# Optimization experiments

Measured on AMD Instinct MI355X. Metric: run time of the kernel, lower is better.

Reference implementation:

```python
import jax, jax.numpy as jnp
import numpy as np

NLAT_IN, NLON_IN = 360, 720
NLAT_OUT, NLON_OUT = 180, 360
KERNEL_SIZE = 3
THETA_CUTOFF = KERNEL_SIZE * np.pi / NLAT_IN  # default theta_cutoff
B, C = 2, 64


def _cc_lats_weights(n):
    # Clenshaw-Curtis quadrature on [-1,1] (torch-harmonics 'equiangular' grid);
    # latitudes (colatitude) = arccos(nodes) = pi*k/(n-1) in [0, pi].
    N = n - 1
    theta = np.pi * np.arange(n) / N
    w = np.ones(n)
    for j in range(1, N // 2 + 1):
        b = 1.0 if 2 * j == N else 2.0
        w -= b * np.cos(2.0 * j * theta) / (4.0 * j * j - 1.0)
    w *= 2.0 / N
    w[0] *= 0.5
    w[-1] *= 0.5
    return theta, w


def _precompute_psi():
    # Mirrors _precompute_convolution_tensor + _compute_support_vals_isotropic.
    d_theta = THETA_CUTOFF / KERNEL_SIZE
    lats_in, _ = _cc_lats_weights(NLAT_IN)
    lats_out, _ = _cc_lats_weights(NLAT_OUT)
    phis = np.linspace(0.0, 2.0 * np.pi, NLON_IN)
    alpha = -lats_in[None, :, None].astype(np.float32)   # [1, H, 1]
    beta = phis[None, None, :].astype(np.float32)        # [1, 1, W]
    gamma = lats_out[:, None, None].astype(np.float32)   # [T, 1, 1]
    z = np.cos(alpha) * np.cos(gamma) - np.cos(beta) * np.sin(alpha) * np.sin(gamma)
    with np.errstate(invalid="ignore"):
        theta = np.arccos(z)  # [T, H, W]; nan where |z|>1 (excluded by mask, as in torch)
    segs, lats, lons, vals = [], [], [], []
    for ik in range(KERNEL_SIZE):
        itheta = ik * d_theta
        with np.errstate(invalid="ignore"):
            mask = (np.abs(theta - itheta) < d_theta) & (theta < THETA_CUTOFF)
        t_idx, h_idx, w_idx = np.nonzero(mask)
        segs.append(ik * NLAT_OUT + t_idx)  # fused (kernel, nlat_out) segment id
        lats.append(h_idx)
        lons.append(w_idx)
        vals.append(1.0 - np.abs(theta[mask] - itheta) / d_theta)
    return (np.concatenate(segs).astype(np.int32),
            np.concatenate(lats).astype(np.int32),
            np.concatenate(lons).astype(np.int32),
            np.concatenate(vals).astype(np.float32))


def setup_inputs() -> dict:
    key = jax.random.key(0)
    x = jax.random.normal(key, (B, C, NLAT_IN, NLON_IN), dtype=jnp.float32)
    _, wgl = _cc_lats_weights(NLAT_IN)
    quad_weights = jnp.asarray(2.0 * np.pi * wgl[:, None] / NLON_IN, dtype=jnp.float32)
    seg, lat, lon, val = _precompute_psi()
    return {"x": x, "quad_weights": quad_weights,
            "psi_seg": jnp.asarray(seg), "psi_lat": jnp.asarray(lat),
            "psi_lon": jnp.asarray(lon), "psi_val": jnp.asarray(val)}


def reference(x, quad_weights, psi_seg, psi_lat, psi_lon, psi_val):
    # out[b,c,k,t,p] = sum_{(k,t,h,w) in psi} val * qw[h] * x[b,c,h,(w-(p+1)*s) mod W]
    Bx, Cx, H, W = x.shape
    scale = W // NLON_OUT  # longitudinal shift per output longitude (torch.roll step)
    xw = (quad_weights * x).reshape(Bx * Cx, H, W)  # [BC, H, W]
    num_seg = KERNEL_SIZE * NLAT_OUT

    def step(carry, p):
        cols = (psi_lon - (p + 1) * scale) % W                 # rolled longitude per nnz
        g = xw[:, psi_lat, cols] * psi_val                     # [BC, nnz] gather + scale
        out_p = jax.ops.segment_sum(g.T, psi_seg, num_segments=num_seg)  # [K*T, BC]
        return carry, out_p

    _, ys = jax.lax.scan(step, None, jnp.arange(NLON_OUT))     # [P, K*T, BC]
    out = ys.transpose(2, 1, 0).reshape(Bx, Cx, KERNEL_SIZE, NLAT_OUT, NLON_OUT)
    return out
```

## Files before the change

### kernel.cpp

```cpp
#include <hip/hip_runtime.h>


#define NLAT_IN  360
#define NLON_IN  720
#define NLAT_OUT 180
#define NLON_OUT 360
#define KSIZE    3
#define NSEG     (KSIZE * NLAT_OUT)
#define CHW      (NLAT_IN * NLON_IN)
#define BCTOT    128
#define G        4
#define NBCG     (BCTOT / G)
#define MAXR     2
#define PH       10
#define NTHREADS 256
#define SLOTS    432
#define MIRROR   (SLOTS - NLON_OUT)
#define ROWB     (SLOTS * 16)

typedef float v2f __attribute__((ext_vector_type(2)));

__device__ __forceinline__ void PKF(v2f& a, v2f x, v2f c) {
    asm("v_pk_fma_f32 %0, %1, %2, %0" : "+v"(a) : "v"(x), "v"(c));
}


__global__ void prep1_kernel(const int* __restrict__ seg, const int* __restrict__ lat,
                             const float* __restrict__ val, int nnz,
                             int* __restrict__ ptrh, int* __restrict__ hbase,
                             int* __restrict__ hlast, int* __restrict__ flags) {
    int idx = blockIdx.x * blockDim.x + threadIdx.x;
    if (idx >= NSEG * PH) return;
    int s = idx / PH, j = idx - s * PH;
    int lo = 0, hi = nnz;
    while (lo < hi) { int m = (lo + hi) >> 1; if (seg[m] < s) lo = m + 1; else hi = m; }
    int e0 = lo;
    lo = e0; hi = nnz;
    while (lo < hi) { int m = (lo + hi) >> 1; if (seg[m] < s + 1) lo = m + 1; else hi = m; }
    int e1 = lo;
    if (e0 >= e1) {
        ptrh[idx] = e0; flags[idx] = 0;
        if (j == 0) { hbase[s] = 1 << 28; hlast[s] = -(1 << 28); }
        return;
    }
    int hb = lat[e0];
    if (j == 0) { hbase[s] = hb; hlast[s] = lat[e1 - 1]; }
    int a;
    { int tg = hb + j; lo = e0; hi = e1;
      while (lo < hi) { int m = (lo + hi) >> 1; if (lat[m] < tg) lo = m + 1; else hi = m; }
      a = lo; }
    ptrh[idx] = a;
    int f = 0;
    if (j < PH - 1) {
        int tg = hb + j + 1; lo = a; hi = e1;
        while (lo < hi) { int m = (lo + hi) >> 1; if (lat[m] < tg) lo = m + 1; else hi = m; }
        int b = lo;
        if (b - a == NLON_IN) {
            float v0 = val[a], v1 = val[a + 240], v2 = val[a + 480];
            float d = fmaxf(fabsf(v0 - v1), fmaxf(fabsf(v0 - v2), fabsf(v1 - v2)));
            f = (d < 1e-5f) ? 1 : 0;
        }
    }
    flags[idx] = f;
}

__global__ void cf_kernel(const int* __restrict__ lat, const float* __restrict__ val,
                          const float* __restrict__ qw, int nnz, float* __restrict__ cfb) {
    int e = blockIdx.x * blockDim.x + threadIdx.x;
    if (e < nnz) cfb[e] = val[e] * qw[lat[e]];
}

__global__ void runs_kernel(const int* __restrict__ lon, const int* __restrict__ ptrh,
                            const int* __restrict__ flags,
                            int* __restrict__ runcnt, uint2* __restrict__ runslab) {
    const int idx  = blockIdx.x * 4 + (threadIdx.x >> 6);
    if (idx >= NSEG * PH) return;
    const int lane = threadIdx.x & 63;
    const int j = idx % PH;
    int runbase = 0;
    if (j < PH - 1) {
        const int a = ptrh[idx], b = ptrh[idx + 1];
        if (b > a && !flags[idx]) {
            for (int c = a; c < b; c += 64) {
                const int e = c + lane;
                const bool active = e < b;
                const int w   = active ? lon[e] : 0;
                const int wm1 = (active && e > a) ? lon[e - 1] : -99;
                const bool isStart = active && (lane == 0 || w != wm1 + 1);
                const unsigned long long mask = __ballot(isStart);
                if (isStart) {
                    const int cnt = min(64, b - c);
                    unsigned long long hv = (mask >> lane) >> 1;
                    const int len = hv ? __ffsll((long long)hv) : (cnt - lane);
                    const int cidx = __popcll(mask & ((1ull << lane) - 1ull));
                    const int s0 = ((w >> 1) + NLON_OUT - 1) % NLON_OUT;
                    runslab[a + runbase + cidx] = make_uint2(
                        (unsigned)e, (unsigned)(s0 | ((w & 1) << 9) | (len << 11)));
                }
                runbase += __popcll(mask);
            }
        }
    }
    if (lane == 0) runcnt[idx] = runbase;
}


__global__ __launch_bounds__(NTHREADS) void disco_kernel(
    const float* __restrict__ x,
    const float* __restrict__ cfb,
    const uint2* __restrict__ runslab,
    const int*   __restrict__ runcnt,
    const int*   __restrict__ ptrh,
    const int*   __restrict__ hbase,
    const int*   __restrict__ hlast,
    const int*   __restrict__ flags,
    float*       __restrict__ out)
{
    __shared__ float4 ldsx[MAXR * 2][SLOTS];
    __shared__ v2f    accbuf[120][6];

    const int tid      = threadIdx.x;
    const int lane     = tid & 63;
    const int wpair    = tid >> 7;
    const int pairlane = tid & 127;
    const int pid      = (pairlane < 120) ? pairlane : pairlane - 120;
    const int p0       = 3 * pid;
    const int bc0      = blockIdx.x * G;
    const int ty       = blockIdx.y;
    const int t        = (ty & 1) ? (NLAT_OUT - 1 - (ty >> 1)) : (ty >> 1);
    const int s        = blockIdx.z * NLAT_OUT + t;
    const int hb = hbase[s], hl = hlast[s];

    v2f a0l = {0.f, 0.f}, a0h = a0l, a1l = a0l, a1h = a0l, a2l = a0l, a2h = a0l;
    const char* lb = (const char*)&ldsx[0][0];

    for (int r0 = hb; r0 <= hl; r0 += MAXR) {
        const int rn = min(MAXR, hl - r0 + 1);
        __syncthreads();
        for (int r = 0; r < rn; ++r) {
            const float* xr = x + (size_t)bc0 * CHW + (size_t)(r0 + r) * NLON_IN;
            for (int m = tid; m < NLON_OUT; m += NTHREADS) {
                const float2 v0 = *(const float2*)(xr + 2 * m);
                const float2 v1 = *(const float2*)(xr + 2 * m + CHW);
                const float2 v2 = *(const float2*)(xr + 2 * m + 2 * CHW);
                const float2 v3 = *(const float2*)(xr + 2 * m + 3 * CHW);
                const float4 ev = {v0.x, v1.x, v2.x, v3.x};
                const float4 ov = {v0.y, v1.y, v2.y, v3.y};
                ldsx[2 * r + 0][m] = ev;
                ldsx[2 * r + 1][m] = ov;
                if (m < MIRROR) {
                    ldsx[2 * r + 0][NLON_OUT + m] = ev;
                    ldsx[2 * r + 1][NLON_OUT + m] = ov;
                }
            }
        }
        __syncthreads();
        for (int r = 0; r < rn; ++r) {
            const int j = (r0 + r) - hb;
            if (j < 0 || j >= PH - 1) continue;
            if ((j & 1) != wpair) continue;
            const int idx = s * PH + j;
            const int a = ptrh[idx], b = ptrh[idx + 1];
            if (a >= b) continue;
            const int rp0 = (j & 1) * 2;
            if (flags[idx]) {
                float4 v = {0.f, 0.f, 0.f, 0.f};
                for (int m = lane; m < NLON_OUT; m += 64) {
                    const float4 u0 = ldsx[rp0][m], u1 = ldsx[rp0 + 1][m];
                    v.x += u0.x + u1.x; v.y += u0.y + u1.y;
                    v.z += u0.z + u1.z; v.w += u0.w + u1.w;
                }
#pragma unroll
                for (int o = 32; o >= 1; o >>= 1) {
                    v.x += __shfl_xor(v.x, o); v.y += __shfl_xor(v.y, o);
                    v.z += __shfl_xor(v.z, o); v.w += __shfl_xor(v.w, o);
                }
                const float cf = cfb[a];
                a0l.x = fmaf(cf, v.x, a0l.x); a0l.y = fmaf(cf, v.y, a0l.y);
                a0h.x = fmaf(cf, v.z, a0h.x); a0h.y = fmaf(cf, v.w, a0h.y);
                a1l.x = fmaf(cf, v.x, a1l.x); a1l.y = fmaf(cf, v.y, a1l.y);
                a1h.x = fmaf(cf, v.z, a1h.x); a1h.y = fmaf(cf, v.w, a1h.y);
                a2l.x = fmaf(cf, v.x, a2l.x); a2l.y = fmaf(cf, v.y, a2l.y);
                a2h.x = fmaf(cf, v.z, a2h.x); a2h.y = fmaf(cf, v.w, a2h.y);
                continue;
            }
            const int rc = runcnt[idx];
            for (int rr = 0; rr < rc; ++rr) {
                const uint2 R = runslab[a + rr];
                const int e0  = __builtin_amdgcn_readfirstlane((int)R.x);
                const int y   = __builtin_amdgcn_readfirstlane((int)R.y);
                const int s0A = y & 511;
                const int odd = (y >> 9) & 1;
                const int len = y >> 11;
                int qA = s0A - p0 - 2; qA += (qA >> 31) & NLON_OUT;
                const char* baseA = lb + (size_t)(rp0 + odd) * ROWB + ((size_t)qA << 4);
                const char* baseB = lb + (size_t)(rp0 + (odd ^ 1)) * ROWB
                                       + ((size_t)(qA + odd) << 4);
                const float* cfp = cfb + e0;
                int i = 0;
                if (len >= 8) {
                    v2f A0l = *(const v2f*)(baseA +  0), A0h = *(const v2f*)(baseA +  8);
                    v2f A1l = *(const v2f*)(baseA + 16), A1h = *(const v2f*)(baseA + 24);
                    v2f A2l = *(const v2f*)(baseA + 32), A2h = *(const v2f*)(baseA + 40);
                    v2f B0l = *(const v2f*)(baseB +  0), B0h = *(const v2f*)(baseB +  8);
                    v2f B1l = *(const v2f*)(baseB + 16), B1h = *(const v2f*)(baseB + 24);
                    v2f B2l = *(const v2f*)(baseB + 32), B2h = *(const v2f*)(baseB + 40);
                    v2f A3l, A3h, B3l, B3h;
                    const char* ldA = baseA + 48;
                    const char* ldB = baseB + 48;
                    for (; i + 8 <= len; i += 8) {
                        float cs; v2f c;
                        A3l = *(const v2f*)(ldA); A3h = *(const v2f*)(ldA + 8); ldA += 16;
                        cs = cfp[i + 0]; c = (v2f){cs, cs};
                        PKF(a2l, A0l, c); PKF(a2h, A0h, c);
                        PKF(a1l, A1l, c); PKF(a1h, A1h, c);
                        PKF(a0l, A2l, c); PKF(a0h, A2h, c);
                        B3l = *(const v2f*)(ldB); B3h = *(const v2f*)(ldB + 8); ldB += 16;
                        cs = cfp[i + 1]; c = (v2f){cs, cs};
                        PKF(a2l, B0l, c); PKF(a2h, B0h, c);
                        PKF(a1l, B1l, c); PKF(a1h, B1h, c);
                        PKF(a0l, B2l, c); PKF(a0h, B2h, c);
                        A0l = *(const v2f*)(ldA); A0h = *(const v2f*)(ldA + 8); ldA += 16;
                        cs = cfp[i + 2]; c = (v2f){cs, cs};
                        PKF(a2l, A1l, c); PKF(a2h, A1h, c);
                        PKF(a1l, A2l, c); PKF(a1h, A2h, c);
                        PKF(a0l, A3l, c); PKF(a0h, A3h, c);
                        B0l = *(const v2f*)(ldB); B0h = *(const v2f*)(ldB + 8); ldB += 16;
                        cs = cfp[i + 3]; c = (v2f){cs, cs};
                        PKF(a2l, B1l, c); PKF(a2h, B1h, c);
                        PKF(a1l, B2l, c); PKF(a1h, B2h, c);
                        PKF(a0l, B3l, c); PKF(a0h, B3h, c);
                        A1l = *(const v2f*)(ldA); A1h = *(const v2f*)(ldA + 8); ldA += 16;
                        cs = cfp[i + 4]; c = (v2f){cs, cs};
                        PKF(a2l, A2l, c); PKF(a2h, A2h, c);
                        PKF(a1l, A3l, c); PKF(a1h, A3h, c);
                        PKF(a0l, A0l, c); PKF(a0h, A0h, c);
                        B1l = *(const v2f*)(ldB); B1h = *(const v2f*)(ldB + 8); ldB += 16;
                        cs = cfp[i + 5]; c = (v2f){cs, cs};
                        PKF(a2l, B2l, c); PKF(a2h, B2h, c);
                        PKF(a1l, B3l, c); PKF(a1h, B3h, c);
                        PKF(a0l, B0l, c); PKF(a0h, B0h, c);
                        A2l = *(const v2f*)(ldA); A2h = *(const v2f*)(ldA + 8); ldA += 16;
                        cs = cfp[i + 6]; c = (v2f){cs, cs};
                        PKF(a2l, A3l, c); PKF(a2h, A3h, c);
                        PKF(a1l, A0l, c); PKF(a1h, A0h, c);
                        PKF(a0l, A1l, c); PKF(a0h, A1h, c);
                        B2l = *(const v2f*)(ldB); B2h = *(const v2f*)(ldB + 8); ldB += 16;
                        cs = cfp[i + 7]; c = (v2f){cs, cs};
                        PKF(a2l, B3l, c); PKF(a2h, B3h, c);
                        PKF(a1l, B0l, c); PKF(a1h, B0h, c);
                        PKF(a0l, B1l, c); PKF(a0h, B1h, c);
                    }
                }
                for (; i < len; ++i) {
                    const int m = i >> 1;
                    const char* bp = (i & 1) ? (baseB + ((size_t)m << 4))
                                             : (baseA + ((size_t)m << 4));
                    const float cs = cfp[i]; const v2f c = (v2f){cs, cs};
                    const v2f w0l = *(const v2f*)(bp +  0), w0h = *(const v2f*)(bp +  8);
                    const v2f w1l = *(const v2f*)(bp + 16), w1h = *(const v2f*)(bp + 24);
                    const v2f w2l = *(const v2f*)(bp + 32), w2h = *(const v2f*)(bp + 40);
                    PKF(a2l, w0l, c); PKF(a2h, w0h, c);
                    PKF(a1l, w1l, c); PKF(a1h, w1h, c);
                    PKF(a0l, w2l, c); PKF(a0h, w2h, c);
                }
            }
        }
    }

    __syncthreads();
    if (wpair == 1 && pairlane < 120) {
        accbuf[pid][0] = a0l; accbuf[pid][1] = a0h;
        accbuf[pid][2] = a1l; accbuf[pid][3] = a1h;
        accbuf[pid][4] = a2l; accbuf[pid][5] = a2h;
    }
    __syncthreads();
    if (wpair == 0 && pairlane < 120) {
        a0l += accbuf[pid][0]; a0h += accbuf[pid][1];
        a1l += accbuf[pid][2]; a1h += accbuf[pid][3];
        a2l += accbuf[pid][4]; a2h += accbuf[pid][5];
        const size_t cs_ = (size_t)NSEG * NLON_OUT;
        const size_t ob  = ((size_t)bc0 * NSEG + s) * NLON_OUT + p0;
        out[ob]              = a0l.x; out[ob + 1]              = a1l.x; out[ob + 2]              = a2l.x;
        out[ob + cs_]        = a0l.y; out[ob + cs_ + 1]        = a1l.y; out[ob + cs_ + 2]        = a2l.y;
        out[ob + 2 * cs_]    = a0h.x; out[ob + 2 * cs_ + 1]    = a1h.x; out[ob + 2 * cs_ + 2]    = a2h.x;
        out[ob + 3 * cs_]    = a0h.y; out[ob + 3 * cs_ + 1]    = a1h.y; out[ob + 3 * cs_ + 2]    = a2h.y;
    }
}


__global__ void segptr_kernel(const int* __restrict__ seg, int nnz, int* __restrict__ ptr) {
    int s = blockIdx.x * blockDim.x + threadIdx.x;
    if (s > NSEG) return;
    if (s == NSEG) { ptr[NSEG] = nnz; return; }
    int lo = 0, hi = nnz;
    while (lo < hi) { int m = (lo + hi) >> 1; if (seg[m] < s) lo = m + 1; else hi = m; }
    ptr[s] = lo;
}

__global__ __launch_bounds__(384) void disco_simple_kernel(
    const float* __restrict__ x, const float* __restrict__ qw,
    const int* __restrict__ lat, const int* __restrict__ lon,
    const float* __restrict__ val, const int* __restrict__ ptr,
    float* __restrict__ out)
{
    const int p = threadIdx.x;
    if (p >= NLON_OUT) return;
    const int kt = blockIdx.x, bc0 = blockIdx.y * 8;
    const int e0 = ptr[kt], e1 = ptr[kt + 1];
    float acc[8];
#pragma unroll
    for (int g = 0; g < 8; ++g) acc[g] = 0.0f;
    const int pw = 2 * p + 2;
    const float* xb = x + (size_t)bc0 * CHW;
    for (int e = e0; e < e1; ++e) {
        const int h = lat[e], w = lon[e];
        const float cf = val[e] * qw[h];
        int col = w - pw; if (col < 0) col += NLON_IN;
        const float* src = xb + h * NLON_IN + col;
#pragma unroll
        for (int g = 0; g < 8; ++g) acc[g] = fmaf(cf, src[(size_t)g * CHW], acc[g]);
    }
    const size_t ob = ((size_t)bc0 * NSEG + kt) * NLON_OUT + p;
#pragma unroll
    for (int g = 0; g < 8; ++g) out[ob + (size_t)g * NSEG * NLON_OUT] = acc[g];
}


extern "C" void kernel_launch(void* const* d_in, const int* in_sizes, int n_in,
                              void* d_out, int out_size, void* d_ws, size_t ws_size,
                              hipStream_t stream)
{
    const float* x   = (const float*)d_in[0];
    const float* qw  = (const float*)d_in[1];
    const int*   seg = (const int*)  d_in[2];
    const int*   lat = (const int*)  d_in[3];
    const int*   lon = (const int*)  d_in[4];
    const float* val = (const float*)d_in[5];
    const int    nnz = in_sizes[2];
    const int    nnzpad = (nnz + 3) & ~3;

    char* w = (char*)d_ws;
    size_t off = 0;
    int* ptrh   = (int*)(w + off); off += (size_t)NSEG * PH * 4;
    int* hbase  = (int*)(w + off); off += NSEG * 4;
    int* hlast  = (int*)(w + off); off += NSEG * 4;
    int* flags  = (int*)(w + off); off += (size_t)NSEG * PH * 4;
    int* runcnt = (int*)(w + off); off += (size_t)NSEG * PH * 4;
    float* cfb  = (float*)(w + off); off += (size_t)nnzpad * 4;
    off = (off + 7) & ~(size_t)7;
    uint2* runslab = (uint2*)(w + off); off += (size_t)nnz * 8;

    if (ws_size < off) {
        int* ptr = (int*)d_ws;
        segptr_kernel<<<(NSEG + 1 + 255) / 256, 256, 0, stream>>>(seg, nnz, ptr);
        dim3 grid(NSEG, BCTOT / 8);
        disco_simple_kernel<<<grid, 384, 0, stream>>>(x, qw, lat, lon, val, ptr,
                                                      (float*)d_out);
        return;
    }

    prep1_kernel<<<(NSEG * PH + 255) / 256, 256, 0, stream>>>(seg, lat, val, nnz,
                                                              ptrh, hbase, hlast, flags);
    cf_kernel<<<(nnz + 255) / 256, 256, 0, stream>>>(lat, val, qw, nnz, cfb);
    runs_kernel<<<(NSEG * PH + 3) / 4, 256, 0, stream>>>(lon, ptrh, flags,
                                                         runcnt, runslab);

    dim3 grid(NBCG, NLAT_OUT, KSIZE);
    disco_kernel<<<grid, NTHREADS, 0, stream>>>(x, cfb, runslab, runcnt,
                                                ptrh, hbase, hlast, flags,
                                                (float*)d_out);
}
```

Baseline: 183.2 us.

## Prefetch next row pair into registers while computing current rows

Global loads of input rows are moved into registers (sv0/sv1/sv2) and issued for the next MAXR row pair before the compute phase on the current pair, then written to LDS after the next barrier. The per-row loop is flattened so 720 elements across two rows are covered by three fixed per-thread slots. This hides global memory latency behind the FMA loop. The cost is extra register pressure from 24 prefetch floats, which may reduce occupancy.

```diff
diff --git a/kernel.cpp b/kernel.cpp
--- a/kernel.cpp
+++ b/kernel.cpp
@@ -17,6 +17,7 @@
 #define SLOTS    432
 #define MIRROR   (SLOTS - NLON_OUT)
 #define ROWB     (SLOTS * 16)
+#define SWI      3
 
 typedef float v2f __attribute__((ext_vector_type(2)));
 
@@ -134,135 +135,200 @@
     v2f a0l = {0.f, 0.f}, a0h = a0l, a1l = a0l, a1h = a0l, a2l = a0l, a2h = a0l;
     const char* lb = (const char*)&ldsx[0][0];
 
-    for (int r0 = hb; r0 <= hl; r0 += MAXR) {
-        const int rn = min(MAXR, hl - r0 + 1);
-        __syncthreads();
-        for (int r = 0; r < rn; ++r) {
-            const float* xr = x + (size_t)bc0 * CHW + (size_t)(r0 + r) * NLON_IN;
-            for (int m = tid; m < NLON_OUT; m += NTHREADS) {
-                const float2 v0 = *(const float2*)(xr + 2 * m);
-                const float2 v1 = *(const float2*)(xr + 2 * m + CHW);
-                const float2 v2 = *(const float2*)(xr + 2 * m + 2 * CHW);
-                const float2 v3 = *(const float2*)(xr + 2 * m + 3 * CHW);
-                const float4 ev = {v0.x, v1.x, v2.x, v3.x};
-                const float4 ov = {v0.y, v1.y, v2.y, v3.y};
-                ldsx[2 * r + 0][m] = ev;
-                ldsx[2 * r + 1][m] = ov;
-                if (m < MIRROR) {
-                    ldsx[2 * r + 0][NLON_OUT + m] = ev;
-                    ldsx[2 * r + 1][NLON_OUT + m] = ov;
+    float2 sv0[4], sv1[4], sv2[4];
+    const float* xb = x + (size_t)bc0 * CHW;
+
+#define LOADW(R0)                                                              \
+    {                                                                          \
+        {   const int idx_ = tid;                     \
+            const int rr_ = idx_ >= 360;                                       \
+            const int m_  = idx_ - 360 * rr_;                                  \
+            const int row_ = min((R0) + rr_, hl);                              \
+            const float* xr_ = xb + (size_t)row_ * NLON_IN + 2 * m_;           \
+            sv0[0] = *(const float2*)(xr_);                                    \
+            sv0[1] = *(const float2*)(xr_ + CHW);                              \
+            sv0[2] = *(const float2*)(xr_ + 2 * CHW);                          \
+            sv0[3] = *(const float2*)(xr_ + 3 * CHW);                          \
+        }                                                                      \
+        {   const int idx_ = tid + 256;               \
+            const int rr_ = idx_ >= 360;                                       \
+            const int m_  = idx_ - 360 * rr_;                                  \
+            const int row_ = min((R0) + rr_, hl);                              \
+            const float* xr_ = xb + (size_t)row_ * NLON_IN + 2 * m_;           \
+            sv1[0] = *(const float2*)(xr_);                                    \
+            sv1[1] = *(const float2*)(xr_ + CHW);                              \
+            sv1[2] = *(const float2*)(xr_ + 2 * CHW);                          \
+            sv1[3] = *(const float2*)(xr_ + 3 * CHW);                          \
+        }                                                                      \
+        if (tid < 208) {                                 \
+            const int idx_ = tid + 512;                                        \
+            const int rr_ = 1;                                                 \
+            const int m_  = idx_ - 360;                                        \
+            const int row_ = min((R0) + rr_, hl);                              \
+            const float* xr_ = xb + (size_t)row_ * NLON_IN + 2 * m_;           \
+            sv2[0] = *(const float2*)(xr_);                                    \
+            sv2[1] = *(const float2*)(xr_ + CHW);                              \
+            sv2[2] = *(const float2*)(xr_ + 2 * CHW);                          \
+            sv2[3] = *(const float2*)(xr_ + 3 * CHW);                          \
+        }                                                                      \
+    }
+
+#define WRITEW()                                                               \
+    {                                                                          \
+        {   const int idx_ = tid;                                              \
+            const int rr_ = idx_ >= 360;                                       \
+            const int m_  = idx_ - 360 * rr_;                                  \
+            const float4 ev_ = {sv0[0].x, sv0[1].x, sv0[2].x, sv0[3].x};       \
+            const float4 ov_ = {sv0[0].y, sv0[1].y, sv0[2].y, sv0[3].y};       \
+            ldsx[2 * rr_ + 0][m_] = ev_;                                       \
+            ldsx[2 * rr_ + 1][m_] = ov_;                                       \
+            if (m_ < MIRROR) {                                                 \
+                ldsx[2 * rr_ + 0][NLON_OUT + m_] = ev_;                        \
+                ldsx[2 * rr_ + 1][NLON_OUT + m_] = ov_;                        \
+            }                                                                  \
+        }                                                                      \
+        {   const int idx_ = tid + 256;                                        \
+            const int rr_ = idx_ >= 360;                                       \
+            const int m_  = idx_ - 360 * rr_;                                  \
+            const float4 ev_ = {sv1[0].x, sv1[1].x, sv1[2].x, sv1[3].x};       \
+            const float4 ov_ = {sv1[0].y, sv1[1].y, sv1[2].y, sv1[3].y};       \
+            ldsx[2 * rr_ + 0][m_] = ev_;                                       \
+            ldsx[2 * rr_ + 1][m_] = ov_;                                       \
+            if (m_ < MIRROR) {                                                 \
+                ldsx[2 * rr_ + 0][NLON_OUT + m_] = ev_;                        \
+                ldsx[2 * rr_ + 1][NLON_OUT + m_] = ov_;                        \
+            }                                                                  \
+        }                                                                      \
+        if (tid < 208) {                                                       \
+            const int m_ = tid + 512 - 360;                                    \
+            const float4 ev_ = {sv2[0].x, sv2[1].x, sv2[2].x, sv2[3].x};       \
+            const float4 ov_ = {sv2[0].y, sv2[1].y, sv2[2].y, sv2[3].y};       \
+            ldsx[2][m_] = ev_;                                                 \
+            ldsx[3][m_] = ov_;                                                 \
+            if (m_ < MIRROR) {                                                 \
+                ldsx[2][NLON_OUT + m_] = ev_;                                  \
+                ldsx[3][NLON_OUT + m_] = ov_;                                  \
+            }                                                                  \
+        }                                                                      \
+    }
+
+    if (hb <= hl) {
+        LOADW(hb);
+        for (int r0 = hb; r0 <= hl; r0 += MAXR) {
+            const int rn = min(MAXR, hl - r0 + 1);
+            __syncthreads();
+            WRITEW();
+            if (r0 + MAXR <= hl) LOADW(r0 + MAXR);
+            __syncthreads();
+            for (int r = 0; r < rn; ++r) {
+                const int j = (r0 + r) - hb;
+                if (j < 0 || j >= PH - 1) continue;
+                if ((j & 1) != wpair) continue;
+                const int idx = s * PH + j;
+                const int a = ptrh[idx], b = ptrh[idx + 1];
+                if (a >= b) continue;
+                const int rp0 = (j & 1) * 2;
+                if (flags[idx]) {
+                    float4 v = {0.f, 0.f, 0.f, 0.f};
+                    for (int m = lane; m < NLON_OUT; m += 64) {
+                        const float4 u0 = ldsx[rp0][m], u1 = ldsx[rp0 + 1][m];
+                        v.x += u0.x + u1.x; v.y += u0.y + u1.y;
+                        v.z += u0.z + u1.z; v.w += u0.w + u1.w;
+                    }
+#pragma unroll
+                    for (int o = 32; o >= 1; o >>= 1) {
+                        v.x += __shfl_xor(v.x, o); v.y += __shfl_xor(v.y, o);
+                        v.z += __shfl_xor(v.z, o); v.w += __shfl_xor(v.w, o);
+                    }
+                    const float cf = cfb[a];
+                    a0l.x = fmaf(cf, v.x, a0l.x); a0l.y = fmaf(cf, v.y, a0l.y);
+                    a0h.x = fmaf(cf, v.z, a0h.x); a0h.y = fmaf(cf, v.w, a0h.y);
+                    a1l.x = fmaf(cf, v.x, a1l.x); a1l.y = fmaf(cf, v.y, a1l.y);
+                    a1h.x = fmaf(cf, v.z, a1h.x); a1h.y = fmaf(cf, v.w, a1h.y);
+                    a2l.x = fmaf(cf, v.x, a2l.x); a2l.y = fmaf(cf, v.y, a2l.y);
+                    a2h.x = fmaf(cf, v.z, a2h.x); a2h.y = fmaf(cf, v.w, a2h.y);
+                    continue;
                 }
-            }
-        }
-        __syncthreads();
-        for (int r = 0; r < rn; ++r) {
-            const int j = (r0 + r) - hb;
-            if (j < 0 || j >= PH - 1) continue;
-            if ((j & 1) != wpair) continue;
-            const int idx = s * PH + j;
-            const int a = ptrh[idx], b = ptrh[idx + 1];
-            if (a >= b) continue;
-            const int rp0 = (j & 1) * 2;
-            if (flags[idx]) {
-                float4 v = {0.f, 0.f, 0.f, 0.f};
-                for (int m = lane; m < NLON_OUT; m += 64) {
-                    const float4 u0 = ldsx[rp0][m], u1 = ldsx[rp0 + 1][m];
-                    v.x += u0.x + u1.x; v.y += u0.y + u1.y;
-                    v.z += u0.z + u1.z; v.w += u0.w + u1.w;
-                }
-#pragma unroll
-                for (int o = 32; o >= 1; o >>= 1) {
-                    v.x += __shfl_xor(v.x, o); v.y += __shfl_xor(v.y, o);
-                    v.z += __shfl_xor(v.z, o); v.w += __shfl_xor(v.w, o);
-                }
-                const float cf = cfb[a];
-                a0l.x = fmaf(cf, v.x, a0l.x); a0l.y = fmaf(cf, v.y, a0l.y);
-                a0h.x = fmaf(cf, v.z, a0h.x); a0h.y = fmaf(cf, v.w, a0h.y);
-                a1l.x = fmaf(cf, v.x, a1l.x); a1l.y = fmaf(cf, v.y, a1l.y);
-                a1h.x = fmaf(cf, v.z, a1h.x); a1h.y = fmaf(cf, v.w, a1h.y);
-                a2l.x = fmaf(cf, v.x, a2l.x); a2l.y = fmaf(cf, v.y, a2l.y);
-                a2h.x = fmaf(cf, v.z, a2h.x); a2h.y = fmaf(cf, v.w, a2h.y);
-                continue;
-            }
-            const int rc = runcnt[idx];
-            for (int rr = 0; rr < rc; ++rr) {
-                const uint2 R = runslab[a + rr];
-                const int e0  = __builtin_amdgcn_readfirstlane((int)R.x);
-                const int y   = __builtin_amdgcn_readfirstlane((int)R.y);
-                const int s0A = y & 511;
-                const int odd = (y >> 9) & 1;
-                const int len = y >> 11;
-                int qA = s0A - p0 - 2; qA += (qA >> 31) & NLON_OUT;
-                const char* baseA = lb + (size_t)(rp0 + odd) * ROWB + ((size_t)qA << 4);
-                const char* baseB = lb + (size_t)(rp0 + (odd ^ 1)) * ROWB
-                                       + ((size_t)(qA + odd) << 4);
-                const float* cfp = cfb + e0;
-                int i = 0;
-                if (len >= 8) {
-                    v2f A0l = *(const v2f*)(baseA +  0), A0h = *(const v2f*)(baseA +  8);
-                    v2f A1l = *(const v2f*)(baseA + 16), A1h = *(const v2f*)(baseA + 24);
-                    v2f A2l = *(const v2f*)(baseA + 32), A2h = *(const v2f*)(baseA + 40);
-                    v2f B0l = *(const v2f*)(baseB +  0), B0h = *(const v2f*)(baseB +  8);
-                    v2f B1l = *(const v2f*)(baseB + 16), B1h = *(const v2f*)(baseB + 24);
-                    v2f B2l = *(const v2f*)(baseB + 32), B2h = *(const v2f*)(baseB + 40);
-                    v2f A3l, A3h, B3l, B3h;
-                    const char* ldA = baseA + 48;
-                    const char* ldB = baseB + 48;
-                    for (; i + 8 <= len; i += 8) {
-                        float cs; v2f c;
-                        A3l = *(const v2f*)(ldA); A3h = *(const v2f*)(ldA + 8); ldA += 16;
-                        cs = cfp[i + 0]; c = (v2f){cs, cs};
-                        PKF(a2l, A0l, c); PKF(a2h, A0h, c);
-                        PKF(a1l, A1l, c); PKF(a1h, A1h, c);
-                        PKF(a0l, A2l, c); PKF(a0h, A2h, c);
-                        B3l = *(const v2f*)(ldB); B3h = *(const v2f*)(ldB + 8); ldB += 16;
-                        cs = cfp[i + 1]; c = (v2f){cs, cs};
-                        PKF(a2l, B0l, c); PKF(a2h, B0h, c);
-                        PKF(a1l, B1l, c); PKF(a1h, B1h, c);
-                        PKF(a0l, B2l, c); PKF(a0h, B2h, c);
-                        A0l = *(const v2f*)(ldA); A0h = *(const v2f*)(ldA + 8); ldA += 16;
-                        cs = cfp[i + 2]; c = (v2f){cs, cs};
-                        PKF(a2l, A1l, c); PKF(a2h, A1h, c);
-                        PKF(a1l, A2l, c); PKF(a1h, A2h, c);
-                        PKF(a0l, A3l, c); PKF(a0h, A3h, c);
-                        B0l = *(const v2f*)(ldB); B0h = *(const v2f*)(ldB + 8); ldB += 16;
-                        cs = cfp[i + 3]; c = (v2f){cs, cs};
-                        PKF(a2l, B1l, c); PKF(a2h, B1h, c);
-                        PKF(a1l, B2l, c); PKF(a1h, B2h, c);
-                        PKF(a0l, B3l, c); PKF(a0h, B3h, c);
-                        A1l = *(const v2f*)(ldA); A1h = *(const v2f*)(ldA + 8); ldA += 16;
-                        cs = cfp[i + 4]; c = (v2f){cs, cs};
-                        PKF(a2l, A2l, c); PKF(a2h, A2h, c);
-                        PKF(a1l, A3l, c); PKF(a1h, A3h, c);
-                        PKF(a0l, A0l, c); PKF(a0h, A0h, c);
-                        B1l = *(const v2f*)(ldB); B1h = *(const v2f*)(ldB + 8); ldB += 16;
-                        cs = cfp[i + 5]; c = (v2f){cs, cs};
-                        PKF(a2l, B2l, c); PKF(a2h, B2h, c);
-                        PKF(a1l, B3l, c); PKF(a1h, B3h, c);
-                        PKF(a0l, B0l, c); PKF(a0h, B0h, c);
-                        A2l = *(const v2f*)(ldA); A2h = *(const v2f*)(ldA + 8); ldA += 16;
-                        cs = cfp[i + 6]; c = (v2f){cs, cs};
-                        PKF(a2l, A3l, c); PKF(a2h, A3h, c);
-                        PKF(a1l, A0l, c); PKF(a1h, A0h, c);
-                        PKF(a0l, A1l, c); PKF(a0h, A1h, c);
-                        B2l = *(const v2f*)(ldB); B2h = *(const v2f*)(ldB + 8); ldB += 16;
-                        cs = cfp[i + 7]; c = (v2f){cs, cs};
-                        PKF(a2l, B3l, c); PKF(a2h, B3h, c);
-                        PKF(a1l, B0l, c); PKF(a1h, B0h, c);
-                        PKF(a0l, B1l, c); PKF(a0h, B1h, c);
+                const int rc = runcnt[idx];
+                for (int rr = 0; rr < rc; ++rr) {
+                    const uint2 R = runslab[a + rr];
+                    const int e0  = __builtin_amdgcn_readfirstlane((int)R.x);
+                    const int y   = __builtin_amdgcn_readfirstlane((int)R.y);
+                    const int s0A = y & 511;
+                    const int odd = (y >> 9) & 1;
+                    const int len = y >> 11;
+                    int qA = s0A - p0 - 2; qA += (qA >> 31) & NLON_OUT;
+                    const char* baseA = lb + (size_t)(rp0 + odd) * ROWB + ((size_t)qA << 4);
+                    const char* baseB = lb + (size_t)(rp0 + (odd ^ 1)) * ROWB
+                                           + ((size_t)(qA + odd) << 4);
+                    const float* cfp = cfb + e0;
+                    int i = 0;
+                    if (len >= 8) {
+                        v2f A0l = *(const v2f*)(baseA +  0), A0h = *(const v2f*)(baseA +  8);
+                        v2f A1l = *(const v2f*)(baseA + 16), A1h = *(const v2f*)(baseA + 24);
+                        v2f A2l = *(const v2f*)(baseA + 32), A2h = *(const v2f*)(baseA + 40);
+                        v2f B0l = *(const v2f*)(baseB +  0), B0h = *(const v2f*)(baseB +  8);
+                        v2f B1l = *(const v2f*)(baseB + 16), B1h = *(const v2f*)(baseB + 24);
+                        v2f B2l = *(const v2f*)(baseB + 32), B2h = *(const v2f*)(baseB + 40);
+                        v2f A3l, A3h, B3l, B3h;
+                        const char* ldA = baseA + 48;
+                        const char* ldB = baseB + 48;
+                        for (; i + 8 <= len; i += 8) {
+                            float cs; v2f c;
+                            A3l = *(const v2f*)(ldA); A3h = *(const v2f*)(ldA + 8); ldA += 16;
+                            cs = cfp[i + 0]; c = (v2f){cs, cs};
+                            PKF(a2l, A0l, c); PKF(a2h, A0h, c);
+                            PKF(a1l, A1l, c); PKF(a1h, A1h, c);
+                            PKF(a0l, A2l, c); PKF(a0h, A2h, c);
+                            B3l = *(const v2f*)(ldB); B3h = *(const v2f*)(ldB + 8); ldB += 16;
+                            cs = cfp[i + 1]; c = (v2f){cs, cs};
+                            PKF(a2l, B0l, c); PKF(a2h, B0h, c);
+                            PKF(a1l, B1l, c); PKF(a1h, B1h, c);
+                            PKF(a0l, B2l, c); PKF(a0h, B2h, c);
+                            A0l = *(const v2f*)(ldA); A0h = *(const v2f*)(ldA + 8); ldA += 16;
+                            cs = cfp[i + 2]; c = (v2f){cs, cs};
+                            PKF(a2l, A1l, c); PKF(a2h, A1h, c);
+                            PKF(a1l, A2l, c); PKF(a1h, A2h, c);
+                            PKF(a0l, A3l, c); PKF(a0h, A3h, c);
+                            B0l = *(const v2f*)(ldB); B0h = *(const v2f*)(ldB + 8); ldB += 16;
+                            cs = cfp[i + 3]; c = (v2f){cs, cs};
+                            PKF(a2l, B1l, c); PKF(a2h, B1h, c);
+                            PKF(a1l, B2l, c); PKF(a1h, B2h, c);
+                            PKF(a0l, B3l, c); PKF(a0h, B3h, c);
+                            A1l = *(const v2f*)(ldA); A1h = *(const v2f*)(ldA + 8); ldA += 16;
+                            cs = cfp[i + 4]; c = (v2f){cs, cs};
+                            PKF(a2l, A2l, c); PKF(a2h, A2h, c);
+                            PKF(a1l, A3l, c); PKF(a1h, A3h, c);
+                            PKF(a0l, A0l, c); PKF(a0h, A0h, c);
+                            B1l = *(const v2f*)(ldB); B1h = *(const v2f*)(ldB + 8); ldB += 16;
+                            cs = cfp[i + 5]; c = (v2f){cs, cs};
+                            PKF(a2l, B2l, c); PKF(a2h, B2h, c);
+                            PKF(a1l, B3l, c); PKF(a1h, B3h, c);
+                            PKF(a0l, B0l, c); PKF(a0h, B0h, c);
+                            A2l = *(const v2f*)(ldA); A2h = *(const v2f*)(ldA + 8); ldA += 16;
+                            cs = cfp[i + 6]; c = (v2f){cs, cs};
+                            PKF(a2l, A3l, c); PKF(a2h, A3h, c);
+                            PKF(a1l, A0l, c); PKF(a1h, A0h, c);
+                            PKF(a0l, A1l, c); PKF(a0h, A1h, c);
+                            B2l = *(const v2f*)(ldB); B2h = *(const v2f*)(ldB + 8); ldB += 16;
+                            cs = cfp[i + 7]; c = (v2f){cs, cs};
+                            PKF(a2l, B3l, c); PKF(a2h, B3h, c);
+                            PKF(a1l, B0l, c); PKF(a1h, B0h, c);
+                            PKF(a0l, B1l, c); PKF(a0h, B1h, c);
+                        }
                     }
-                }
-                for (; i < len; ++i) {
-                    const int m = i >> 1;
-                    const char* bp = (i & 1) ? (baseB + ((size_t)m << 4))
-                                             : (baseA + ((size_t)m << 4));
-                    const float cs = cfp[i]; const v2f c = (v2f){cs, cs};
-                    const v2f w0l = *(const v2f*)(bp +  0), w0h = *(const v2f*)(bp +  8);
-                    const v2f w1l = *(const v2f*)(bp + 16), w1h = *(const v2f*)(bp + 24);
-                    const v2f w2l = *(const v2f*)(bp + 32), w2h = *(const v2f*)(bp + 40);
-                    PKF(a2l, w0l, c); PKF(a2h, w0h, c);
-                    PKF(a1l, w1l, c); PKF(a1h, w1h, c);
-                    PKF(a0l, w2l, c); PKF(a0h, w2h, c);
+                    for (; i < len; ++i) {
+                        const int m = i >> 1;
+                        const char* bp = (i & 1) ? (baseB + ((size_t)m << 4))
+                                                 : (baseA + ((size_t)m << 4));
+                        const float cs = cfp[i]; const v2f c = (v2f){cs, cs};
+                        const v2f w0l = *(const v2f*)(bp +  0), w0h = *(const v2f*)(bp +  8);
+                        const v2f w1l = *(const v2f*)(bp + 16), w1h = *(const v2f*)(bp + 24);
+                        const v2f w2l = *(const v2f*)(bp + 32), w2h = *(const v2f*)(bp + 40);
+                        PKF(a2l, w0l, c); PKF(a2h, w0h, c);
+                        PKF(a1l, w1l, c); PKF(a1h, w1h, c);
+                        PKF(a0l, w2l, c); PKF(a0h, w2h, c);
+                    }
                 }
             }
         }
@@ -286,6 +352,8 @@
         out[ob + 2 * cs_]    = a0h.x; out[ob + 2 * cs_ + 1]    = a1h.x; out[ob + 2 * cs_ + 2]    = a2h.x;
         out[ob + 3 * cs_]    = a0h.y; out[ob + 3 * cs_ + 1]    = a1h.y; out[ob + 3 * cs_ + 2]    = a2h.y;
     }
+#undef LOADW
+#undef WRITEW
 }
 
 
```

Result: faster. 152.9 us (-16.5%).
